# Optimization experiments

Hardware: AMD Instinct MI355X
Metric: run time of the kernel (lower is better)

## Reference

```python
import jax, jax.numpy as jnp
import numpy as np

B, S, D_MODEL = 8, 2048, 512
G, V = 2, 320          # num_groups, num_vars
CV_DIM = 256 // G      # proj_dim // num_groups = 128
TAU = 2.0


def setup_inputs() -> dict:
    key = jax.random.key(0)
    k1, k2, k3, k4, k5 = jax.random.split(key, 5)
    hidden_states = jax.random.normal(k1, (B, S, D_MODEL), dtype=jnp.float32)
    # Linear(d_model -> G*V); store as (in, out) for direct matmul
    W = jax.random.normal(k2, (D_MODEL, G * V), dtype=jnp.float32) * (1.0 / np.sqrt(D_MODEL))
    b = jax.random.normal(k3, (G * V,), dtype=jnp.float32) * 0.01
    codevectors = jax.random.normal(k4, (1, G * V, CV_DIM), dtype=jnp.float32)
    # pre-sampled Gumbel(0,1) noise, shape (B*S*G, V)
    u = jax.random.uniform(k5, (B * S * G, V), dtype=jnp.float32,
                           minval=1e-10, maxval=1.0)
    gumbels = -jnp.log(-jnp.log(u))
    return {"hidden_states": hidden_states, "W": W, "b": b,
            "codevectors": codevectors, "gumbels": gumbels}


def reference(hidden_states, W, b, codevectors, gumbels):
    Bs, Ss, _ = hidden_states.shape
    N = Bs * Ss
    # weight projection: (B,S,D) @ (D,G*V) -> (B,S,G*V)
    logits = hidden_states @ W + b
    logits = logits.reshape(N * G, V).astype(jnp.float32)

    # gumbel-softmax, hard=True with straight-through
    y_soft = jax.nn.softmax((logits + gumbels) / TAU, axis=-1)  # (N*G, V)
    idx = jnp.argmax(y_soft, axis=-1)
    y_hard = jax.nn.one_hot(idx, V, dtype=y_soft.dtype)
    codevector_probs = y_hard - jax.lax.stop_gradient(y_soft) + y_soft

    # perplexity from the (noise-free) soft distribution
    soft_dist = jax.nn.softmax(logits.reshape(N, G, V), axis=-1)
    marginal = soft_dist.mean(axis=0)                            # (G, V)
    perplexity = jnp.exp(-jnp.sum(marginal * jnp.log(marginal + 1e-7),
                                  axis=-1)).sum()

    # codebook lookup as weighted sum (equivalent to one-hot gather)
    cv = codevectors.reshape(G, V, CV_DIM)
    probs = codevector_probs.reshape(N, G, V)
    out = jnp.einsum('ngv,gvd->ngd', probs, cv)                  # (N, G, d)
    out = out.reshape(Bs, Ss, G * CV_DIM)
    return out, perplexity
```

## Files before the change

### kernel.cpp

```cpp
#include <hip/hip_runtime.h>

#define M_ROWS 16384
#define K_DIM  512
#define N_COLS 640
#define V_CODES 320
#define CV_DIM 128

typedef _Float16 half8 __attribute__((ext_vector_type(8)));
typedef _Float16 half4v __attribute__((ext_vector_type(4)));
typedef float floatx4 __attribute__((ext_vector_type(4)));

__device__ inline void gll16(const void* g, void* l) {
    __builtin_amdgcn_global_load_lds(
        (const __attribute__((address_space(1))) void*)g,
        (__attribute__((address_space(3))) void*)l, 16, 0, 0);
}

#define SBAR()  __builtin_amdgcn_sched_barrier(0)
#define WAITV(N) asm volatile("s_waitcnt vmcnt(" #N ")" ::: "memory")
#define WAITL() asm volatile("s_waitcnt lgkmcnt(0)" ::: "memory")

__global__ __launch_bounds__(256)
void prepW(const float* __restrict__ W, _Float16* __restrict__ Wt,
           float* __restrict__ marginal) {
    __shared__ float tile[32][33];
    const int b = blockIdx.x, t = threadIdx.x;
    if (b == 320) {
        for (int i = t; i < 640; i += 256) marginal[i] = 0.f;
        return;
    }
    const int n0 = (b % 20) * 32, k0 = (b / 20) * 32;
    {
        const int kk = t >> 3, nn4 = (t & 7) << 2;
        const float4 w = *(const float4*)(W + (size_t)(k0 + kk) * 640 + n0 + nn4);
        tile[kk][nn4 + 0] = w.x; tile[kk][nn4 + 1] = w.y;
        tile[kk][nn4 + 2] = w.z; tile[kk][nn4 + 3] = w.w;
    }
    __syncthreads();
    {
        const int nn = t >> 3, kk4 = (t & 7) << 2;
        half4v h = {(_Float16)tile[kk4 + 0][nn], (_Float16)tile[kk4 + 1][nn],
                    (_Float16)tile[kk4 + 2][nn], (_Float16)tile[kk4 + 3][nn]};
        *(half4v*)(Wt + (size_t)(n0 + nn) * 512 + k0 + kk4) = h;
    }
}

__global__ __launch_bounds__(256, 2)
void fused(const float* __restrict__ A, const _Float16* __restrict__ Bt,
           const float* __restrict__ bias, const float* __restrict__ gum,
           const float* __restrict__ cv, float* __restrict__ out,
           float* __restrict__ marginal) {
    __shared__ _Float16 Bs[2][320 * 32];
    __shared__ _Float16 As[2][64 * 32];
    __shared__ float smarg[320];
    const int t = threadIdx.x;
    const int wave = t >> 6, lane = t & 63;
    const int bm = blockIdx.x, g = blockIdx.y;
    const int mi = wave;
    const int c = lane & 15, kq = lane >> 4;

    for (int i = t; i < 320; i += 256) smarg[i] = 0.f;

    floatx4 acc[20];
#pragma unroll
    for (int nt = 0; nt < 20; ++nt) acc[nt] = (floatx4){0.f, 0.f, 0.f, 0.f};

    const int am = t >> 2, ad = t & 3;
    const int a_wr = am * 64 + ((ad ^ (am & 3)) << 4);
    const float* Aptr = A + (size_t)(bm * 64 + am) * 512 + ad * 8;

    const _Float16* Bg = Bt + (size_t)g * V_CODES * K_DIM;

    float4 avA0, avA1;
    float4 avN0, avN1;

    auto ISSUE_B = [&](int buf, int k0) {
#pragma unroll
        for (int s = 0; s < 5; ++s) {
            const int q = t + 256 * s;
            const int n = q >> 2, j = q & 3;
            gll16(Bg + (size_t)n * 512 + k0 + ((j ^ (n & 3)) << 3),
                  (char*)(&Bs[buf][0]) + q * 16);
        }
    };
    auto WRITE_A = [&](int buf, const float4& v0, const float4& v1) {
        const half8 h = {(_Float16)v0.x, (_Float16)v0.y, (_Float16)v0.z,
                         (_Float16)v0.w, (_Float16)v1.x, (_Float16)v1.y,
                         (_Float16)v1.z, (_Float16)v1.w};
        *(half8*)((char*)(&As[buf][0]) + a_wr) = h;
    };
    auto COMPUTE = [&](int cur) {
        const int ra = mi * 16 + c;
        const half8 af = *(const half8*)((const char*)(&As[cur][0]) +
                          ra * 64 + ((kq ^ (ra & 3)) << 4));
        __builtin_amdgcn_s_setprio(1);
#pragma unroll
        for (int nt = 0; nt < 20; ++nt) {
            const int rb = nt * 16 + c;
            const half8 bf = *(const half8*)((const char*)(&Bs[cur][0]) +
                              rb * 64 + ((kq ^ (rb & 3)) << 4));
            acc[nt] = __builtin_amdgcn_mfma_f32_16x16x32_f16(af, bf, acc[nt], 0, 0, 0);
        }
        __builtin_amdgcn_s_setprio(0);
    };

    avA0 = *(const float4*)(Aptr + 0);
    avA1 = *(const float4*)(Aptr + 4);
    ISSUE_B(0, 0);
    WRITE_A(0, avA0, avA1);
    avA0 = *(const float4*)(Aptr + 32);
    avA1 = *(const float4*)(Aptr + 36);
    ISSUE_B(1, 32);
    SBAR(); WAITV(7);
    SBAR(); WAITL();
    SBAR(); __builtin_amdgcn_s_barrier(); SBAR();

    for (int kt = 0; kt < 14; ++kt) {
        const int cur = kt & 1;
        COMPUTE(cur);
        SBAR(); __builtin_amdgcn_s_barrier(); SBAR();
        avN0 = *(const float4*)(Aptr + (kt + 2) * 32);
        avN1 = *(const float4*)(Aptr + (kt + 2) * 32 + 4);
        ISSUE_B(cur, (kt + 2) * 32);
        WRITE_A(cur ^ 1, avA0, avA1);
        SBAR(); WAITV(7);
        SBAR(); WAITL();
        SBAR(); __builtin_amdgcn_s_barrier(); SBAR();
        avA0 = avN0; avA1 = avN1;
    }
    COMPUTE(0);
    SBAR(); __builtin_amdgcn_s_barrier(); SBAR();
    WRITE_A(1, avA0, avA1);
    SBAR(); WAITV(0);
    SBAR(); WAITL();
    SBAR(); __builtin_amdgcn_s_barrier(); SBAR();
    COMPUTE(1);

    float bcol[20];
#pragma unroll
    for (int nt = 0; nt < 20; ++nt) bcol[nt] = bias[g * V_CODES + nt * 16 + c];

    float mcontrib[20];
#pragma unroll
    for (int nt = 0; nt < 20; ++nt) mcontrib[nt] = 0.f;

#pragma unroll
    for (int rg = 0; rg < 4; ++rg) {
        const int ntok = bm * 64 + mi * 16 + kq * 4 + rg;
        float lg[20];
#pragma unroll
        for (int nt = 0; nt < 20; ++nt) lg[nt] = acc[nt][rg] + bcol[nt];
        const float* gr = gum + ((size_t)ntok * 2 + g) * V_CODES + c;
        float gv[20];
#pragma unroll
        for (int nt = 0; nt < 20; ++nt) gv[nt] = gr[nt * 16];
        float best = -1e30f; int bidx = 0;
#pragma unroll
        for (int nt = 0; nt < 20; ++nt) {
            const float nz = lg[nt] + gv[nt];
            const int v = nt * 16 + c;
            if (nz > best) { best = nz; bidx = v; }
        }
#pragma unroll
        for (int mask = 1; mask <= 8; mask <<= 1) {
            const float ob = __shfl_xor(best, mask);
            const int   oi = __shfl_xor(bidx, mask);
            if (ob > best || (ob == best && oi < bidx)) { best = ob; bidx = oi; }
        }
        float s = 0.f;
#pragma unroll
        for (int nt = 0; nt < 20; ++nt) { lg[nt] = __expf(lg[nt]); s += lg[nt]; }
#pragma unroll
        for (int mask = 1; mask <= 8; mask <<= 1) s += __shfl_xor(s, mask);
        const float inv = 1.f / s;
#pragma unroll
        for (int nt = 0; nt < 20; ++nt) mcontrib[nt] += lg[nt] * inv;
        const float4* cvp = (const float4*)(cv + ((size_t)g * V_CODES + bidx) * CV_DIM)
                            + c * 2;
        const float4 v0 = cvp[0], v1 = cvp[1];
        float4* op = (float4*)(out + (size_t)ntok * 256 + g * CV_DIM) + c * 2;
        op[0] = v0; op[1] = v1;
    }

#pragma unroll
    for (int nt = 0; nt < 20; ++nt) {
        mcontrib[nt] += __shfl_xor(mcontrib[nt], 16);
        mcontrib[nt] += __shfl_xor(mcontrib[nt], 32);
    }
    if (lane < 16) {
#pragma unroll
        for (int nt = 0; nt < 20; ++nt)
            atomicAdd(&smarg[nt * 16 + c], mcontrib[nt]);
    }
    __syncthreads();
    for (int i = t; i < 320; i += 256)
        atomicAdd(marginal + g * V_CODES + i, smarg[i]);
}

__global__ __launch_bounds__(640)
void finalize(const float* __restrict__ marginal, float* __restrict__ perp_out) {
    __shared__ float terms[640];
    __shared__ float gsum[2];
    const int t = threadIdx.x;

    const float m = marginal[t] * (1.0f / (float)M_ROWS);
    terms[t] = -m * __logf(m + 1e-7f);
    __syncthreads();

    if (t < 128) {
        const int g = t >> 6, lane = t & 63;
        float e = 0.f;
#pragma unroll
        for (int j = 0; j < 5; ++j) e += terms[g * V_CODES + lane + 64 * j];
#pragma unroll
        for (int off = 32; off; off >>= 1) e += __shfl_down(e, off);
        if (lane == 0) gsum[g] = e;
    }
    __syncthreads();
    if (t == 0) perp_out[0] = __expf(gsum[0]) + __expf(gsum[1]);
}

extern "C" void kernel_launch(void* const* d_in, const int* in_sizes, int n_in,
                              void* d_out, int out_size, void* d_ws, size_t ws_size,
                              hipStream_t stream) {
    (void)in_sizes; (void)n_in; (void)out_size; (void)ws_size;
    const float* hs = (const float*)d_in[0];
    const float* W  = (const float*)d_in[1];
    const float* bi = (const float*)d_in[2];
    const float* cv = (const float*)d_in[3];
    const float* gu = (const float*)d_in[4];
    float* out = (float*)d_out;

    _Float16* Wt       = (_Float16*)d_ws;
    float*    marginal = (float*)(Wt + (size_t)N_COLS * K_DIM);

    prepW<<<321, 256, 0, stream>>>(W, Wt, marginal);
    fused<<<dim3(256, 2), 256, 0, stream>>>(hs, Wt, bi, gu, cv, out, marginal);
    finalize<<<1, 640, 0, stream>>>(marginal, out + (size_t)M_ROWS * 256);
}
```

Measured before the change: 48.48 us.

## Split wave tiles 2x2 across M and N and reduce epilogue through shared memory

Waves now tile the 64x320 block as 2 M-tiles by 10 N-tiles each instead of 1 by 20. Each B fragment read from LDS then feeds two MFMAs, which halves B LDS traffic per MFMA. Because each row's softmax and argmax is now split across two waves, partial max, index and sum are combined through shared memory with extra barriers. The codebook gather is done by half the waves using wider stores.

```diff
diff --git a/kernel.cpp b/kernel.cpp
--- a/kernel.cpp
+++ b/kernel.cpp
@@ -53,17 +53,25 @@
     __shared__ _Float16 Bs[2][320 * 32];
     __shared__ _Float16 As[2][64 * 32];
     __shared__ float smarg[320];
+    __shared__ float wbest[2][64];
+    __shared__ float wsum[2][64];
+    __shared__ int   wbidx[2][64];
+    __shared__ int   fbidx[64];
+    __shared__ float finv[64];
+
     const int t = threadIdx.x;
     const int wave = t >> 6, lane = t & 63;
     const int bm = blockIdx.x, g = blockIdx.y;
-    const int mi = wave;
+    const int mi = wave >> 1, nh = wave & 1;
     const int c = lane & 15, kq = lane >> 4;
 
     for (int i = t; i < 320; i += 256) smarg[i] = 0.f;
 
-    floatx4 acc[20];
-#pragma unroll
-    for (int nt = 0; nt < 20; ++nt) acc[nt] = (floatx4){0.f, 0.f, 0.f, 0.f};
+    floatx4 acc[2][10];
+#pragma unroll
+    for (int mt = 0; mt < 2; ++mt)
+#pragma unroll
+        for (int nt = 0; nt < 10; ++nt) acc[mt][nt] = (floatx4){0.f, 0.f, 0.f, 0.f};
 
     const int am = t >> 2, ad = t & 3;
     const int a_wr = am * 64 + ((ad ^ (am & 3)) << 4);
@@ -90,16 +98,23 @@
         *(half8*)((char*)(&As[buf][0]) + a_wr) = h;
     };
     auto COMPUTE = [&](int cur) {
-        const int ra = mi * 16 + c;
-        const half8 af = *(const half8*)((const char*)(&As[cur][0]) +
-                          ra * 64 + ((kq ^ (ra & 3)) << 4));
+        half8 af[2];
+#pragma unroll
+        for (int mt = 0; mt < 2; ++mt) {
+            const int ra = mi * 32 + mt * 16 + c;
+            af[mt] = *(const half8*)((const char*)(&As[cur][0]) +
+                      ra * 64 + ((kq ^ (ra & 3)) << 4));
+        }
         __builtin_amdgcn_s_setprio(1);
 #pragma unroll
-        for (int nt = 0; nt < 20; ++nt) {
-            const int rb = nt * 16 + c;
+        for (int nt = 0; nt < 10; ++nt) {
+            const int rb = nh * 160 + nt * 16 + c;
             const half8 bf = *(const half8*)((const char*)(&Bs[cur][0]) +
                               rb * 64 + ((kq ^ (rb & 3)) << 4));
-            acc[nt] = __builtin_amdgcn_mfma_f32_16x16x32_f16(af, bf, acc[nt], 0, 0, 0);
+            acc[0][nt] = __builtin_amdgcn_mfma_f32_16x16x32_f16(af[0], bf,
+                                                                acc[0][nt], 0, 0, 0);
+            acc[1][nt] = __builtin_amdgcn_mfma_f32_16x16x32_f16(af[1], bf,
+                                                                acc[1][nt], 0, 0, 0);
         }
         __builtin_amdgcn_s_setprio(0);
     };
@@ -136,65 +151,100 @@
     SBAR(); __builtin_amdgcn_s_barrier(); SBAR();
     COMPUTE(1);
 
-    float bcol[20];
-#pragma unroll
-    for (int nt = 0; nt < 20; ++nt) bcol[nt] = bias[g * V_CODES + nt * 16 + c];
-
-    float mcontrib[20];
-#pragma unroll
-    for (int nt = 0; nt < 20; ++nt) mcontrib[nt] = 0.f;
-
-#pragma unroll
-    for (int rg = 0; rg < 4; ++rg) {
-        const int ntok = bm * 64 + mi * 16 + kq * 4 + rg;
-        float lg[20];
-#pragma unroll
-        for (int nt = 0; nt < 20; ++nt) lg[nt] = acc[nt][rg] + bcol[nt];
-        const float* gr = gum + ((size_t)ntok * 2 + g) * V_CODES + c;
-        float gv[20];
-#pragma unroll
-        for (int nt = 0; nt < 20; ++nt) gv[nt] = gr[nt * 16];
-        float best = -1e30f; int bidx = 0;
-#pragma unroll
-        for (int nt = 0; nt < 20; ++nt) {
-            const float nz = lg[nt] + gv[nt];
-            const int v = nt * 16 + c;
-            if (nz > best) { best = nz; bidx = v; }
-        }
-#pragma unroll
-        for (int mask = 1; mask <= 8; mask <<= 1) {
-            const float ob = __shfl_xor(best, mask);
-            const int   oi = __shfl_xor(bidx, mask);
-            if (ob > best || (ob == best && oi < bidx)) { best = ob; bidx = oi; }
-        }
-        float s = 0.f;
-#pragma unroll
-        for (int nt = 0; nt < 20; ++nt) { lg[nt] = __expf(lg[nt]); s += lg[nt]; }
-#pragma unroll
-        for (int mask = 1; mask <= 8; mask <<= 1) s += __shfl_xor(s, mask);
-        const float inv = 1.f / s;
-#pragma unroll
-        for (int nt = 0; nt < 20; ++nt) mcontrib[nt] += lg[nt] * inv;
-        const float4* cvp = (const float4*)(cv + ((size_t)g * V_CODES + bidx) * CV_DIM)
-                            + c * 2;
-        const float4 v0 = cvp[0], v1 = cvp[1];
-        float4* op = (float4*)(out + (size_t)ntok * 256 + g * CV_DIM) + c * 2;
-        op[0] = v0; op[1] = v1;
-    }
-
-#pragma unroll
-    for (int nt = 0; nt < 20; ++nt) {
-        mcontrib[nt] += __shfl_xor(mcontrib[nt], 16);
-        mcontrib[nt] += __shfl_xor(mcontrib[nt], 32);
+    float bcol[10];
+#pragma unroll
+    for (int nt = 0; nt < 10; ++nt)
+        bcol[nt] = bias[g * V_CODES + nh * 160 + nt * 16 + c];
+
+#pragma unroll
+    for (int mt = 0; mt < 2; ++mt) {
+#pragma unroll
+        for (int rg = 0; rg < 4; ++rg) {
+            const int row = mi * 32 + mt * 16 + kq * 4 + rg;
+            const float* gr = gum + ((size_t)(bm * 64 + row) * 2 + g) * V_CODES
+                              + nh * 160 + c;
+            float lg[10];
+#pragma unroll
+            for (int nt = 0; nt < 10; ++nt) lg[nt] = acc[mt][nt][rg] + bcol[nt];
+            float best = -1e30f; int bidx = 0;
+#pragma unroll
+            for (int nt = 0; nt < 10; ++nt) {
+                const float nz = lg[nt] + gr[nt * 16];
+                const int v = nh * 160 + nt * 16 + c;
+                if (nz > best) { best = nz; bidx = v; }
+            }
+#pragma unroll
+            for (int mask = 1; mask <= 8; mask <<= 1) {
+                const float ob = __shfl_xor(best, mask);
+                const int   oi = __shfl_xor(bidx, mask);
+                if (ob > best || (ob == best && oi < bidx)) { best = ob; bidx = oi; }
+            }
+            float s = 0.f;
+#pragma unroll
+            for (int nt = 0; nt < 10; ++nt) {
+                const float e = __expf(lg[nt]);
+                acc[mt][nt][rg] = e;
+                s += e;
+            }
+#pragma unroll
+            for (int mask = 1; mask <= 8; mask <<= 1) s += __shfl_xor(s, mask);
+            if (c == 0) {
+                wbest[nh][row] = best;
+                wbidx[nh][row] = bidx;
+                wsum[nh][row]  = s;
+            }
+        }
+    }
+    __syncthreads();
+
+    if (t < 64) {
+        const float b0 = wbest[0][t]; const int i0 = wbidx[0][t];
+        const float b1 = wbest[1][t]; const int i1 = wbidx[1][t];
+        fbidx[t] = (b1 > b0 || (b1 == b0 && i1 < i0)) ? i1 : i0;
+        finv[t]  = 1.f / (wsum[0][t] + wsum[1][t]);
+    }
+    __syncthreads();
+
+    float mcon[10];
+#pragma unroll
+    for (int nt = 0; nt < 10; ++nt) mcon[nt] = 0.f;
+#pragma unroll
+    for (int mt = 0; mt < 2; ++mt) {
+#pragma unroll
+        for (int rg = 0; rg < 4; ++rg) {
+            const float iv = finv[mi * 32 + mt * 16 + kq * 4 + rg];
+#pragma unroll
+            for (int nt = 0; nt < 10; ++nt) mcon[nt] += acc[mt][nt][rg] * iv;
+        }
+    }
+#pragma unroll
+    for (int nt = 0; nt < 10; ++nt) {
+        mcon[nt] += __shfl_xor(mcon[nt], 16);
+        mcon[nt] += __shfl_xor(mcon[nt], 32);
     }
     if (lane < 16) {
 #pragma unroll
-        for (int nt = 0; nt < 20; ++nt)
-            atomicAdd(&smarg[nt * 16 + c], mcontrib[nt]);
+        for (int nt = 0; nt < 10; ++nt)
+            atomicAdd(&smarg[nh * 160 + nt * 16 + c], mcon[nt]);
     }
     __syncthreads();
     for (int i = t; i < 320; i += 256)
         atomicAdd(marginal + g * V_CODES + i, smarg[i]);
+
+    if (nh == 0) {
+#pragma unroll
+        for (int rr = 0; rr < 4; ++rr) {
+            const int row = mi * 32 + rr * 8 + (lane >> 3);
+            const int bi = fbidx[row];
+            const int p = lane & 7;
+            const float4* cvp = (const float4*)(cv +
+                ((size_t)g * V_CODES + bi) * CV_DIM) + p * 4;
+            const float4 v0 = cvp[0], v1 = cvp[1], v2 = cvp[2], v3 = cvp[3];
+            float4* op = (float4*)(out + (size_t)(bm * 64 + row) * 256
+                                   + g * CV_DIM) + p * 4;
+            op[0] = v0; op[1] = v1; op[2] = v2; op[3] = v3;
+        }
+    }
 }
 
 __global__ __launch_bounds__(640)
```

New measurement: 50.49 us. +4.1%, slower.

## Triple-buffer GEMM K-loop and prefetch Gumbel noise across epilogue row groups

Applied to the files above, without the earlier changes.

Converts the fp16 MFMA K-loop from double to triple buffering with rotating LDS pointers. Each step now issues the global-to-LDS B loads and A writes for a later tile before waiting and computing the current one, so loads stay in flight across the compute. The epilogue also prefetches the next row group's Gumbel noise while the current row group runs its argmax and softmax. This uses more LDS (about 46KB per block) and more registers, which may reduce occupancy below the two blocks per CU requested.

```diff
diff --git a/kernel.cpp b/kernel.cpp
--- a/kernel.cpp
+++ b/kernel.cpp
@@ -50,8 +50,8 @@
            const float* __restrict__ bias, const float* __restrict__ gum,
            const float* __restrict__ cv, float* __restrict__ out,
            float* __restrict__ marginal) {
-    __shared__ _Float16 Bs[2][320 * 32];
-    __shared__ _Float16 As[2][64 * 32];
+    __shared__ _Float16 Bs[3][320 * 32];
+    __shared__ _Float16 As[3][64 * 32];
     __shared__ float smarg[320];
     const int t = threadIdx.x;
     const int wave = t >> 6, lane = t & 63;
@@ -74,67 +74,72 @@
     float4 avA0, avA1;
     float4 avN0, avN1;
 
-    auto ISSUE_B = [&](int buf, int k0) {
+    auto ISSUE_B = [&](char* bbase, int k0) {
 #pragma unroll
         for (int s = 0; s < 5; ++s) {
             const int q = t + 256 * s;
             const int n = q >> 2, j = q & 3;
             gll16(Bg + (size_t)n * 512 + k0 + ((j ^ (n & 3)) << 3),
-                  (char*)(&Bs[buf][0]) + q * 16);
-        }
-    };
-    auto WRITE_A = [&](int buf, const float4& v0, const float4& v1) {
+                  bbase + q * 16);
+        }
+    };
+    auto WRITE_A = [&](char* abase, const float4& v0, const float4& v1) {
         const half8 h = {(_Float16)v0.x, (_Float16)v0.y, (_Float16)v0.z,
                          (_Float16)v0.w, (_Float16)v1.x, (_Float16)v1.y,
                          (_Float16)v1.z, (_Float16)v1.w};
-        *(half8*)((char*)(&As[buf][0]) + a_wr) = h;
-    };
-    auto COMPUTE = [&](int cur) {
+        *(half8*)(abase + a_wr) = h;
+    };
+    auto COMPUTE = [&](const char* abase, const char* bbase) {
         const int ra = mi * 16 + c;
-        const half8 af = *(const half8*)((const char*)(&As[cur][0]) +
-                          ra * 64 + ((kq ^ (ra & 3)) << 4));
+        const half8 af = *(const half8*)(abase + ra * 64 + ((kq ^ (ra & 3)) << 4));
         __builtin_amdgcn_s_setprio(1);
 #pragma unroll
         for (int nt = 0; nt < 20; ++nt) {
             const int rb = nt * 16 + c;
-            const half8 bf = *(const half8*)((const char*)(&Bs[cur][0]) +
-                              rb * 64 + ((kq ^ (rb & 3)) << 4));
+            const half8 bf = *(const half8*)(bbase + rb * 64 + ((kq ^ (rb & 3)) << 4));
             acc[nt] = __builtin_amdgcn_mfma_f32_16x16x32_f16(af, bf, acc[nt], 0, 0, 0);
         }
         __builtin_amdgcn_s_setprio(0);
     };
+
+    char *cB = (char*)&Bs[0][0], *wB = (char*)&Bs[1][0], *iB = (char*)&Bs[2][0];
+    char *cA = (char*)&As[0][0], *wA = (char*)&As[1][0], *iA = (char*)&As[2][0];
 
     avA0 = *(const float4*)(Aptr + 0);
     avA1 = *(const float4*)(Aptr + 4);
-    ISSUE_B(0, 0);
-    WRITE_A(0, avA0, avA1);
-    avA0 = *(const float4*)(Aptr + 32);
-    avA1 = *(const float4*)(Aptr + 36);
-    ISSUE_B(1, 32);
+    ISSUE_B(cB, 0);
+    avN0 = *(const float4*)(Aptr + 32);
+    avN1 = *(const float4*)(Aptr + 36);
+    ISSUE_B(wB, 32);
+    WRITE_A(cA, avA0, avA1);
+    avA0 = avN0; avA1 = avN1;
+
+    for (int kt = 0; kt < 14; ++kt) {
+        avN0 = *(const float4*)(Aptr + (kt + 2) * 32);
+        avN1 = *(const float4*)(Aptr + (kt + 2) * 32 + 4);
+        ISSUE_B(iB, (kt + 2) * 32);
+        WRITE_A(wA, avA0, avA1);
+        SBAR(); WAITV(14);
+        SBAR(); WAITL();
+        SBAR(); __builtin_amdgcn_s_barrier(); SBAR();
+        COMPUTE(cA, cB);
+        SBAR(); __builtin_amdgcn_s_barrier(); SBAR();
+        avA0 = avN0; avA1 = avN1;
+        { char* tmp = cB; cB = wB; wB = iB; iB = tmp; }
+        { char* tmp = cA; cA = wA; wA = iA; iA = tmp; }
+    }
+    WRITE_A(wA, avA0, avA1);
     SBAR(); WAITV(7);
     SBAR(); WAITL();
     SBAR(); __builtin_amdgcn_s_barrier(); SBAR();
-
-    for (int kt = 0; kt < 14; ++kt) {
-        const int cur = kt & 1;
-        COMPUTE(cur);
-        SBAR(); __builtin_amdgcn_s_barrier(); SBAR();
-        avN0 = *(const float4*)(Aptr + (kt + 2) * 32);
-        avN1 = *(const float4*)(Aptr + (kt + 2) * 32 + 4);
-        ISSUE_B(cur, (kt + 2) * 32);
-        WRITE_A(cur ^ 1, avA0, avA1);
-        SBAR(); WAITV(7);
-        SBAR(); WAITL();
-        SBAR(); __builtin_amdgcn_s_barrier(); SBAR();
-        avA0 = avN0; avA1 = avN1;
-    }
-    COMPUTE(0);
+    COMPUTE(cA, cB);
     SBAR(); __builtin_amdgcn_s_barrier(); SBAR();
-    WRITE_A(1, avA0, avA1);
+    { char* tmp = cB; cB = wB; wB = iB; iB = tmp; }
+    { char* tmp = cA; cA = wA; wA = iA; iA = tmp; }
     SBAR(); WAITV(0);
     SBAR(); WAITL();
     SBAR(); __builtin_amdgcn_s_barrier(); SBAR();
-    COMPUTE(1);
+    COMPUTE(cA, cB);
 
     float bcol[20];
 #pragma unroll
@@ -144,20 +149,29 @@
 #pragma unroll
     for (int nt = 0; nt < 20; ++nt) mcontrib[nt] = 0.f;
 
-#pragma unroll
-    for (int rg = 0; rg < 4; ++rg) {
+    float gva[20], gvb[20];
+    {
+        const float* gr = gum + ((size_t)(bm * 64 + mi * 16 + kq * 4 + 0) * 2 + g)
+                          * V_CODES + c;
+#pragma unroll
+        for (int nt = 0; nt < 20; ++nt) gva[nt] = gr[nt * 16];
+    }
+
+    auto DO_RG = [&](int rg, float (&gvc)[20], float (&gvn)[20], bool pf) {
+        if (pf) {
+            const float* gr = gum + ((size_t)(bm * 64 + mi * 16 + kq * 4 + rg + 1) * 2
+                              + g) * V_CODES + c;
+#pragma unroll
+            for (int nt = 0; nt < 20; ++nt) gvn[nt] = gr[nt * 16];
+        }
         const int ntok = bm * 64 + mi * 16 + kq * 4 + rg;
         float lg[20];
 #pragma unroll
         for (int nt = 0; nt < 20; ++nt) lg[nt] = acc[nt][rg] + bcol[nt];
-        const float* gr = gum + ((size_t)ntok * 2 + g) * V_CODES + c;
-        float gv[20];
-#pragma unroll
-        for (int nt = 0; nt < 20; ++nt) gv[nt] = gr[nt * 16];
         float best = -1e30f; int bidx = 0;
 #pragma unroll
         for (int nt = 0; nt < 20; ++nt) {
-            const float nz = lg[nt] + gv[nt];
+            const float nz = lg[nt] + gvc[nt];
             const int v = nt * 16 + c;
             if (nz > best) { best = nz; bidx = v; }
         }
@@ -180,7 +194,11 @@
         const float4 v0 = cvp[0], v1 = cvp[1];
         float4* op = (float4*)(out + (size_t)ntok * 256 + g * CV_DIM) + c * 2;
         op[0] = v0; op[1] = v1;
-    }
+    };
+    DO_RG(0, gva, gvb, true);
+    DO_RG(1, gvb, gva, true);
+    DO_RG(2, gva, gvb, true);
+    DO_RG(3, gvb, gva, false);
 
 #pragma unroll
     for (int nt = 0; nt < 20; ++nt) {
```

Result: slower. 49.69 us (+2.5%).

## Transpose MFMA accumulator layout so each lane owns one token's contiguous columns

Applied to the files above, without the earlier changes.

Swaps the MFMA operands so each lane's accumulator holds four consecutive vocab columns of a single token rather than four tokens for one column. The epilogue is rewritten to match: bias and Gumbel noise load as float4, the argmax needs only two cross-lane steps, and each lane copies a larger contiguous slice of the selected codevector. The aim is fewer and wider global loads in the noise-bound epilogue. The cost is that the marginal reduction now needs four shuffles per element and far more LDS atomics.

```diff
diff --git a/kernel.cpp b/kernel.cpp
--- a/kernel.cpp
+++ b/kernel.cpp
@@ -99,7 +99,7 @@
             const int rb = nt * 16 + c;
             const half8 bf = *(const half8*)((const char*)(&Bs[cur][0]) +
                               rb * 64 + ((kq ^ (rb & 3)) << 4));
-            acc[nt] = __builtin_amdgcn_mfma_f32_16x16x32_f16(af, bf, acc[nt], 0, 0, 0);
+            acc[nt] = __builtin_amdgcn_mfma_f32_16x16x32_f16(bf, af, acc[nt], 0, 0, 0);
         }
         __builtin_amdgcn_s_setprio(0);
     };
@@ -136,65 +136,75 @@
     SBAR(); __builtin_amdgcn_s_barrier(); SBAR();
     COMPUTE(1);
 
-    float bcol[20];
-#pragma unroll
-    for (int nt = 0; nt < 20; ++nt) bcol[nt] = bias[g * V_CODES + nt * 16 + c];
-
-    float mcontrib[20];
-#pragma unroll
-    for (int nt = 0; nt < 20; ++nt) mcontrib[nt] = 0.f;
-
-#pragma unroll
-    for (int rg = 0; rg < 4; ++rg) {
-        const int ntok = bm * 64 + mi * 16 + kq * 4 + rg;
-        float lg[20];
-#pragma unroll
-        for (int nt = 0; nt < 20; ++nt) lg[nt] = acc[nt][rg] + bcol[nt];
-        const float* gr = gum + ((size_t)ntok * 2 + g) * V_CODES + c;
-        float gv[20];
-#pragma unroll
-        for (int nt = 0; nt < 20; ++nt) gv[nt] = gr[nt * 16];
-        float best = -1e30f; int bidx = 0;
-#pragma unroll
-        for (int nt = 0; nt < 20; ++nt) {
-            const float nz = lg[nt] + gv[nt];
-            const int v = nt * 16 + c;
-            if (nz > best) { best = nz; bidx = v; }
-        }
-#pragma unroll
-        for (int mask = 1; mask <= 8; mask <<= 1) {
-            const float ob = __shfl_xor(best, mask);
-            const int   oi = __shfl_xor(bidx, mask);
-            if (ob > best || (ob == best && oi < bidx)) { best = ob; bidx = oi; }
-        }
-        float s = 0.f;
-#pragma unroll
-        for (int nt = 0; nt < 20; ++nt) { lg[nt] = __expf(lg[nt]); s += lg[nt]; }
-#pragma unroll
-        for (int mask = 1; mask <= 8; mask <<= 1) s += __shfl_xor(s, mask);
-        const float inv = 1.f / s;
-#pragma unroll
-        for (int nt = 0; nt < 20; ++nt) mcontrib[nt] += lg[nt] * inv;
-        const float4* cvp = (const float4*)(cv + ((size_t)g * V_CODES + bidx) * CV_DIM)
-                            + c * 2;
-        const float4 v0 = cvp[0], v1 = cvp[1];
-        float4* op = (float4*)(out + (size_t)ntok * 256 + g * CV_DIM) + c * 2;
-        op[0] = v0; op[1] = v1;
-    }
-
-#pragma unroll
-    for (int nt = 0; nt < 20; ++nt) {
-        mcontrib[nt] += __shfl_xor(mcontrib[nt], 16);
-        mcontrib[nt] += __shfl_xor(mcontrib[nt], 32);
-    }
-    if (lane < 16) {
-#pragma unroll
-        for (int nt = 0; nt < 20; ++nt)
-            atomicAdd(&smarg[nt * 16 + c], mcontrib[nt]);
+    const size_t ntok = (size_t)bm * 64 + mi * 16 + c;
+    const float* gr = gum + (ntok * 2 + g) * V_CODES;
+    const float* br = bias + g * V_CODES;
+
+#pragma unroll
+    for (int nt = 0; nt < 20; ++nt) {
+        const float4 bv = *(const float4*)(br + nt * 16 + kq * 4);
+        acc[nt][0] += bv.x; acc[nt][1] += bv.y;
+        acc[nt][2] += bv.z; acc[nt][3] += bv.w;
+    }
+
+    float best = -1e30f; int bidx = 0;
+#pragma unroll
+    for (int nt = 0; nt < 20; ++nt) {
+        const float4 gvv = *(const float4*)(gr + nt * 16 + kq * 4);
+        const int v0 = nt * 16 + kq * 4;
+        float nz;
+        nz = acc[nt][0] + gvv.x; if (nz > best) { best = nz; bidx = v0; }
+        nz = acc[nt][1] + gvv.y; if (nz > best) { best = nz; bidx = v0 + 1; }
+        nz = acc[nt][2] + gvv.z; if (nz > best) { best = nz; bidx = v0 + 2; }
+        nz = acc[nt][3] + gvv.w; if (nz > best) { best = nz; bidx = v0 + 3; }
+    }
+#pragma unroll
+    for (int mask = 16; mask <= 32; mask <<= 1) {
+        const float ob = __shfl_xor(best, mask);
+        const int   oi = __shfl_xor(bidx, mask);
+        if (ob > best || (ob == best && oi < bidx)) { best = ob; bidx = oi; }
+    }
+
+    float s = 0.f;
+#pragma unroll
+    for (int nt = 0; nt < 20; ++nt) {
+#pragma unroll
+        for (int rg = 0; rg < 4; ++rg) {
+            const float e = __expf(acc[nt][rg]);
+            acc[nt][rg] = e;
+            s += e;
+        }
+    }
+    s += __shfl_xor(s, 16);
+    s += __shfl_xor(s, 32);
+    const float inv = 1.f / s;
+
+#pragma unroll
+    for (int nt = 0; nt < 20; ++nt) {
+#pragma unroll
+        for (int rg = 0; rg < 4; ++rg) {
+            float v = acc[nt][rg] * inv;
+            v += __shfl_xor(v, 1);
+            v += __shfl_xor(v, 2);
+            v += __shfl_xor(v, 4);
+            v += __shfl_xor(v, 8);
+            if (c == 0) atomicAdd(&smarg[nt * 16 + kq * 4 + rg], v);
+        }
     }
     __syncthreads();
     for (int i = t; i < 320; i += 256)
         atomicAdd(marginal + g * V_CODES + i, smarg[i]);
+
+    {
+        const float4* cvp = (const float4*)(cv + ((size_t)g * V_CODES + bidx) * CV_DIM)
+                            + kq * 8;
+        float4* op = (float4*)(out + ntok * 256 + g * CV_DIM) + kq * 8;
+        float4 vv[8];
+#pragma unroll
+        for (int i = 0; i < 8; ++i) vv[i] = cvp[i];
+#pragma unroll
+        for (int i = 0; i < 8; ++i) op[i] = vv[i];
+    }
 }
 
 __global__ __launch_bounds__(640)
```

After: 58.67 us. 21.0% more time.
